# Kernel optimization log

Measured on AMD Instinct MI355X. Metric: run time of the kernel, lower is better.

Reference implementation:

```python
import jax, jax.numpy as jnp
import numpy as np

IN_F, OUT_F = 4096, 4096

def setup_inputs() -> dict:
    key = jax.random.key(0)
    k1, k2, k3, k4 = jax.random.split(key, 4)
    input = jax.random.normal(k1, (4, 2048, IN_F), dtype=jnp.float32)
    int8_weights = jax.random.randint(k2, (OUT_F, IN_F), -128, 127, dtype=jnp.int8)
    scales = jax.random.normal(k3, (OUT_F,), dtype=jnp.float32)
    bias = jax.random.normal(k4, (1, OUT_F), dtype=jnp.float32)
    return {"input": input, "int8_weights": int8_weights, "scales": scales, "bias": bias}

def reference(input, int8_weights, scales, bias):
    # dequant-then-GEMM, matching F.linear(input, W.to(dtype)) * scales + bias
    w = int8_weights.astype(input.dtype)            # [out, in]
    out = jnp.einsum('bsi,oi->bso', input, w)       # [B, S, out]
    out = out * scales                              # per-output-channel scale
    out = out + bias                                # bias broadcasts [1, out]
    return out
```

## Files before the change

kernel.cpp:

```cpp
#include <hip/hip_runtime.h>
#include <stdint.h>

typedef int   i32x4 __attribute__((ext_vector_type(4)));
typedef float f32x4 __attribute__((ext_vector_type(4)));
typedef _Float16 half8 __attribute__((ext_vector_type(8)));

#define M_DIM 8192
#define N_DIM 4096
#define K_DIM 4096
#define BM 256
#define BN 256
#define BK 64
#define NT (K_DIM / BK)
#define TILE_I8 16384

#define GLOAD_LDS16(g, l)                                        \
    __builtin_amdgcn_global_load_lds(                            \
        (const __attribute__((address_space(1))) uint32_t*)(g),  \
        (__attribute__((address_space(3))) uint32_t*)(l), 16, 0, 0)

#define BARRIER()  asm volatile("s_barrier" ::: "memory")
#define WAIT_VM0() asm volatile("s_waitcnt vmcnt(0)" ::: "memory")

__device__ __forceinline__ int img_off(int row, int slot) {
    return row * 64 + ((slot ^ ((row >> 1) & 3)) << 4);
}

__global__ __launch_bounds__(256)
void prep_a(const float* __restrict__ A, signed char* __restrict__ Apack,
            float* __restrict__ Ascale) {
    const int wv   = threadIdx.x >> 6;
    const int lane = threadIdx.x & 63;
    const int r    = blockIdx.x * 4 + wv;
    const float* row = A + (size_t)r * K_DIM;

    float mx = 0.f;
#pragma unroll
    for (int p = 0; p < 16; ++p) {
        float4 v = *(const float4*)(row + p * 256 + lane * 4);
        mx = fmaxf(mx, fmaxf(fmaxf(fabsf(v.x), fabsf(v.y)),
                             fmaxf(fabsf(v.z), fabsf(v.w))));
    }
#pragma unroll
    for (int s = 1; s < 64; s <<= 1)
        mx = fmaxf(mx, __shfl_xor(mx, s, 64));

    float inv = mx > 0.f ? 127.f / mx : 0.f;
    if (lane == 0) Ascale[r] = mx * (1.f / 127.f);

    const int bm = r >> 8, rl = r & 255;
    signed char* tb = Apack + (size_t)bm * NT * TILE_I8;
#pragma unroll
    for (int g = 0; g < 4; ++g) {
        int col0 = g * 1024 + lane * 16;
        unsigned w[4];
#pragma unroll
        for (int q = 0; q < 4; ++q) {
            float4 v = *(const float4*)(row + col0 + q * 4);
            int a0 = (int)rintf(v.x * inv);
            int a1 = (int)rintf(v.y * inv);
            int a2 = (int)rintf(v.z * inv);
            int a3 = (int)rintf(v.w * inv);
            w[q] = (a0 & 255) | ((a1 & 255) << 8) | ((a2 & 255) << 16)
                 | ((unsigned)(a3 & 255) << 24);
        }
        int kt = col0 >> 6, k = col0 & 63;
        uint4 pk = make_uint4(w[0], w[1], w[2], w[3]);
        *(uint4*)(tb + (size_t)kt * TILE_I8 + img_off(rl, k >> 4)) = pk;
    }
}

__global__ __launch_bounds__(256)
void prep_w(const void* __restrict__ Wv, signed char* __restrict__ Wpack) {
    const int* wp = (const int*)Wv;
    bool wi32 = true;
#pragma unroll
    for (int i = 0; i < 16; ++i) {
        int v = wp[i];
        wi32 = wi32 && (v >= -128 && v <= 127);
    }
    int g = blockIdx.x * 256 + threadIdx.x;
    int r = g >> 8;
    int col0 = (g & 255) << 4;
    uint4 pk;
    if (wi32) {
        const int* p = (const int*)Wv + (size_t)r * K_DIM + col0;
        unsigned w[4];
#pragma unroll
        for (int q = 0; q < 4; ++q) {
            int4 v = *(const int4*)(p + q * 4);
            w[q] = (v.x & 255) | ((v.y & 255) << 8) | ((v.z & 255) << 16)
                 | ((unsigned)(v.w & 255) << 24);
        }
        pk = make_uint4(w[0], w[1], w[2], w[3]);
    } else {
        pk = *(const uint4*)((const signed char*)Wv + (size_t)r * K_DIM + col0);
    }
    int bn = r >> 8, rl = r & 255;
    int kt = col0 >> 6, k = col0 & 63;
    *(uint4*)(Wpack + (size_t)(bn * NT + kt) * TILE_I8 + img_off(rl, k >> 4)) = pk;
}

__global__ __launch_bounds__(512, 2)
void w8a16_gemm_i8(const signed char* __restrict__ Apack,
                   const signed char* __restrict__ Wpack,
                   const float* __restrict__ Ascale,
                   const float* __restrict__ scales,
                   const float* __restrict__ bias,
                   float* __restrict__ out) {
    __shared__ char smem[65536];

    const int tid  = threadIdx.x;
    const int lane = tid & 63;
    const int wv   = tid >> 6;
    const int wm   = wv >> 2;
    const int wn   = wv & 3;
    const int r16  = lane & 15;
    const int kq   = lane >> 4;

    int bid = blockIdx.x;
    int swz = (bid & 7) * 64 + (bid >> 3);
    int bm = swz >> 4;
    int bn = swz & 15;

    const char* Abase = (const char*)Apack + (size_t)bm * NT * TILE_I8 + tid * 16;
    const char* Bbase = (const char*)Wpack + (size_t)bn * NT * TILE_I8 + tid * 16;

    auto issueT = [&](int kt_src, int buf) {
        const char* ga = Abase + (size_t)kt_src * TILE_I8;
        const char* gb = Bbase + (size_t)kt_src * TILE_I8;
        char* la = smem + buf * 32768 + tid * 16;
        char* lb = la + 16384;
        GLOAD_LDS16(ga,        la);
        GLOAD_LDS16(ga + 8192, la + 8192);
        GLOAD_LDS16(gb,        lb);
        GLOAD_LDS16(gb + 8192, lb + 8192);
    };

    i32x4 af[4], bf[4];
    i32x4 acc[8][4] = {};

    auto loadA = [&](int buf, int mh) {
#pragma unroll
        for (int m = 0; m < 4; ++m) {
            int row = wm * 128 + mh * 64 + m * 16 + r16;
            af[m] = *(const i32x4*)(smem + buf * 32768 + img_off(row, kq));
        }
    };
    auto loadB = [&](int buf) {
#pragma unroll
        for (int n = 0; n < 4; ++n) {
            int row = wn * 64 + n * 16 + r16;
            bf[n] = *(const i32x4*)(smem + buf * 32768 + 16384 + img_off(row, kq));
        }
    };
    auto mmac4 = [&](i32x4 (*ac)[4]) {
#pragma unroll
        for (int n = 0; n < 4; ++n)
#pragma unroll
            for (int m = 0; m < 4; ++m)
                ac[m][n] = __builtin_amdgcn_mfma_i32_16x16x64_i8(af[m], bf[n], ac[m][n], 0, 0, 0);
    };

    issueT(0, 0);
    WAIT_VM0();
    BARRIER();

#pragma unroll 1
    for (int t = 0; t < NT; ++t) {
        int buf  = t & 1;
        int nbuf = buf ^ 1;

        if (t + 1 < NT) issueT(t + 1, nbuf);

        loadA(buf, 0);
        loadB(buf);
        __builtin_amdgcn_s_setprio(1);
        mmac4(&acc[0]);
        __builtin_amdgcn_s_setprio(0);

        loadA(buf, 1);
        __builtin_amdgcn_s_setprio(1);
        mmac4(&acc[4]);
        __builtin_amdgcn_s_setprio(0);

        WAIT_VM0();
        BARRIER();
    }

    float sc[4], bs[4];
#pragma unroll
    for (int n = 0; n < 4; ++n) {
        int col = bn * BN + wn * 64 + n * 16 + r16;
        sc[n] = scales[col];
        bs[n] = bias[col];
    }
#pragma unroll
    for (int mi = 0; mi < 8; ++mi) {
        int row0 = bm * BM + wm * 128 + mi * 16 + kq * 4;
#pragma unroll
        for (int j = 0; j < 4; ++j) {
            int row = row0 + j;
            float as_ = Ascale[row];
#pragma unroll
            for (int n = 0; n < 4; ++n) {
                int col = bn * BN + wn * 64 + n * 16 + r16;
                out[(size_t)row * N_DIM + col] =
                    (float)acc[mi][n][j] * (as_ * sc[n]) + bs[n];
            }
        }
    }
}

__global__ __launch_bounds__(256, 2)
void w8a16_gemm(const float* __restrict__ A,
                const void* __restrict__ Wv,
                const float* __restrict__ scales,
                const float* __restrict__ bias,
                float* __restrict__ out) {
    __shared__ char smem[2 * 128 * 64 * 2];
    char* Ash = smem;
    char* Bsh = smem + 128 * 64 * 2;

    const int* wprobe = (const int*)Wv;
    bool wi32 = true;
#pragma unroll
    for (int i = 0; i < 16; ++i) {
        int v = wprobe[i];
        wi32 = wi32 && (v >= -128 && v <= 127);
    }

    const int tid  = threadIdx.x;
    const int lane = tid & 63;
    const int wv   = tid >> 6;
    const int wwm  = wv >> 1;
    const int wwn  = wv & 1;
    const int r16  = lane & 15;
    const int kq   = lane >> 4;
    const int swzl = (r16 & 7) << 4;

    int bid = blockIdx.x;
    int swz = (bid & 7) * 256 + (bid >> 3);
    int bm = swz / 32;
    int bn = swz % 32;

    const int row_a0 = bm * 128;
    const int row_b0 = bn * 128;

    int cr[4], cc[4];
#pragma unroll
    for (int i = 0; i < 4; ++i) {
        int c = tid + 256 * i;
        cr[i] = c >> 3;
        cc[i] = (c & 7) << 3;
    }

    float4 pa[8];
    int4   pbi[8];
    uint2  pb8[4];

    auto load_tile = [&](int kt) {
        int k0 = kt * 64;
#pragma unroll
        for (int i = 0; i < 4; ++i) {
            const float* p = A + (size_t)(row_a0 + cr[i]) * K_DIM + k0 + cc[i];
            pa[2 * i]     = *(const float4*)p;
            pa[2 * i + 1] = *(const float4*)(p + 4);
        }
        if (wi32) {
            const int* w = (const int*)Wv;
#pragma unroll
            for (int i = 0; i < 4; ++i) {
                const int* p = w + (size_t)(row_b0 + cr[i]) * K_DIM + k0 + cc[i];
                pbi[2 * i]     = *(const int4*)p;
                pbi[2 * i + 1] = *(const int4*)(p + 4);
            }
        } else {
            const signed char* w = (const signed char*)Wv;
#pragma unroll
            for (int i = 0; i < 4; ++i) {
                const signed char* p = w + (size_t)(row_b0 + cr[i]) * K_DIM + k0 + cc[i];
                pb8[i] = *(const uint2*)p;
            }
        }
    };

    auto write_lds = [&]() {
#pragma unroll
        for (int i = 0; i < 4; ++i) {
            int off = (cr[i] * 128 + cc[i] * 2) ^ ((cr[i] & 7) << 4);
            half8 h;
            h[0] = (_Float16)pa[2 * i].x;
            h[1] = (_Float16)pa[2 * i].y;
            h[2] = (_Float16)pa[2 * i].z;
            h[3] = (_Float16)pa[2 * i].w;
            h[4] = (_Float16)pa[2 * i + 1].x;
            h[5] = (_Float16)pa[2 * i + 1].y;
            h[6] = (_Float16)pa[2 * i + 1].z;
            h[7] = (_Float16)pa[2 * i + 1].w;
            *(half8*)(Ash + off) = h;

            half8 g;
            if (wi32) {
                g[0] = (_Float16)pbi[2 * i].x;
                g[1] = (_Float16)pbi[2 * i].y;
                g[2] = (_Float16)pbi[2 * i].z;
                g[3] = (_Float16)pbi[2 * i].w;
                g[4] = (_Float16)pbi[2 * i + 1].x;
                g[5] = (_Float16)pbi[2 * i + 1].y;
                g[6] = (_Float16)pbi[2 * i + 1].z;
                g[7] = (_Float16)pbi[2 * i + 1].w;
            } else {
                unsigned x = pb8[i].x, y = pb8[i].y;
                g[0] = (_Float16)(int)(signed char)(x & 0xff);
                g[1] = (_Float16)(int)(signed char)((x >> 8) & 0xff);
                g[2] = (_Float16)(int)(signed char)((x >> 16) & 0xff);
                g[3] = (_Float16)(int)(signed char)(x >> 24);
                g[4] = (_Float16)(int)(signed char)(y & 0xff);
                g[5] = (_Float16)(int)(signed char)((y >> 8) & 0xff);
                g[6] = (_Float16)(int)(signed char)((y >> 16) & 0xff);
                g[7] = (_Float16)(int)(signed char)(y >> 24);
            }
            *(half8*)(Bsh + off) = g;
        }
    };

    f32x4 acc[4][4] = {};

    auto compute = [&]() {
#pragma unroll
        for (int ks = 0; ks < 2; ++ks) {
            half8 af[4], bfr[4];
#pragma unroll
            for (int m = 0; m < 4; ++m) {
                int row = wwm * 64 + m * 16 + r16;
                af[m] = *(const half8*)(Ash + ((row * 128 + ks * 64 + kq * 16) ^ swzl));
            }
#pragma unroll
            for (int n = 0; n < 4; ++n) {
                int row = wwn * 64 + n * 16 + r16;
                bfr[n] = *(const half8*)(Bsh + ((row * 128 + ks * 64 + kq * 16) ^ swzl));
            }
#pragma unroll
            for (int m = 0; m < 4; ++m)
#pragma unroll
                for (int n = 0; n < 4; ++n)
                    acc[m][n] = __builtin_amdgcn_mfma_f32_16x16x32_f16(af[m], bfr[n], acc[m][n], 0, 0, 0);
        }
    };

    load_tile(0);
#pragma unroll 1
    for (int kt = 0; kt < NT; ++kt) {
        if (kt) __syncthreads();
        write_lds();
        __syncthreads();
        if (kt + 1 < NT) load_tile(kt + 1);
        compute();
    }

#pragma unroll
    for (int n = 0; n < 4; ++n) {
        int col = row_b0 + wwn * 64 + n * 16 + r16;
        float s = scales[col];
        float b = bias[col];
#pragma unroll
        for (int m = 0; m < 4; ++m) {
            int row0 = row_a0 + wwm * 64 + m * 16 + kq * 4;
#pragma unroll
            for (int j = 0; j < 4; ++j) {
                out[(size_t)(row0 + j) * N_DIM + col] = acc[m][n][j] * s + b;
            }
        }
    }
}

extern "C" void kernel_launch(void* const* d_in, const int* in_sizes, int n_in,
                              void* d_out, int out_size, void* d_ws, size_t ws_size,
                              hipStream_t stream) {
    const float* A      = (const float*)d_in[0];
    const void*  W      = d_in[1];
    const float* scales = (const float*)d_in[2];
    const float* bias   = (const float*)d_in[3];
    float*       out    = (float*)d_out;

    const size_t needA = (size_t)M_DIM * K_DIM;
    const size_t needW = (size_t)N_DIM * K_DIM;
    const size_t needS = (size_t)M_DIM * sizeof(float);

    if (ws_size >= needA + needW + needS) {
        signed char* Apack = (signed char*)d_ws;
        signed char* Wpack = (signed char*)d_ws + needA;
        float*       Asc   = (float*)((char*)d_ws + needA + needW);
        hipLaunchKernelGGL(prep_a, dim3(2048), dim3(256), 0, stream, A, Apack, Asc);
        hipLaunchKernelGGL(prep_w, dim3(4096), dim3(256), 0, stream, W, Wpack);
        hipLaunchKernelGGL(w8a16_gemm_i8, dim3(512), dim3(512), 0, stream,
                           Apack, Wpack, Asc, scales, bias, out);
    } else {
        hipLaunchKernelGGL(w8a16_gemm, dim3(2048), dim3(256), 0, stream,
                           A, W, scales, bias, out);
    }
}
```

Measured before the change: 200.2 us.

## Load int8 weight fragments straight to registers and shrink GEMM tile to 256x128

Changes the int8 GEMM tile from 256x256 with 8 waves to 256x128 with 4 waves. The weight fragments are now loaded directly from global memory into registers in an MFMA-friendly packed layout, produced by a reworked prep_w. Only the activations are staged through LDS, with double buffering and B registers prefetched one step ahead. The intent is to halve LDS traffic and footprint and raise the block count. The trade-off is more global reads of A, since each A tile is now read by twice as many column blocks, plus higher register pressure from two B fragment sets and eight A fragments.

```diff
diff --git a/kernel.cpp b/kernel.cpp
--- a/kernel.cpp
+++ b/kernel.cpp
@@ -8,11 +8,9 @@
 #define M_DIM 8192
 #define N_DIM 4096
 #define K_DIM 4096
-#define BM 256
-#define BN 256
-#define BK 64
-#define NT (K_DIM / BK)
-#define TILE_I8 16384
+#define NT 64
+#define TILE_A 16384
+#define TILE_B 8192
 
 #define GLOAD_LDS16(g, l)                                        \
     __builtin_amdgcn_global_load_lds(                            \
@@ -49,7 +47,7 @@
     if (lane == 0) Ascale[r] = mx * (1.f / 127.f);
 
     const int bm = r >> 8, rl = r & 255;
-    signed char* tb = Apack + (size_t)bm * NT * TILE_I8;
+    signed char* tb = Apack + (size_t)bm * NT * TILE_A;
 #pragma unroll
     for (int g = 0; g < 4; ++g) {
         int col0 = g * 1024 + lane * 16;
@@ -66,7 +64,7 @@
         }
         int kt = col0 >> 6, k = col0 & 63;
         uint4 pk = make_uint4(w[0], w[1], w[2], w[3]);
-        *(uint4*)(tb + (size_t)kt * TILE_I8 + img_off(rl, k >> 4)) = pk;
+        *(uint4*)(tb + (size_t)kt * TILE_A + img_off(rl, k >> 4)) = pk;
     }
 }
 
@@ -96,115 +94,114 @@
     } else {
         pk = *(const uint4*)((const signed char*)Wv + (size_t)r * K_DIM + col0);
     }
-    int bn = r >> 8, rl = r & 255;
+    int bn = r >> 7, rl = r & 127;
     int kt = col0 >> 6, k = col0 & 63;
-    *(uint4*)(Wpack + (size_t)(bn * NT + kt) * TILE_I8 + img_off(rl, k >> 4)) = pk;
-}
-
-__global__ __launch_bounds__(512, 2)
+    *(uint4*)(Wpack + ((size_t)(bn * NT + kt) * 128 + rl) * 64 + k) = pk;
+}
+
+__global__ __launch_bounds__(256, 2)
 void w8a16_gemm_i8(const signed char* __restrict__ Apack,
                    const signed char* __restrict__ Wpack,
                    const float* __restrict__ Ascale,
                    const float* __restrict__ scales,
                    const float* __restrict__ bias,
                    float* __restrict__ out) {
-    __shared__ char smem[65536];
+    __shared__ char smem[32768];
 
     const int tid  = threadIdx.x;
     const int lane = tid & 63;
     const int wv   = tid >> 6;
-    const int wm   = wv >> 2;
-    const int wn   = wv & 3;
+    const int wm   = wv >> 1;
+    const int wn   = wv & 1;
     const int r16  = lane & 15;
     const int kq   = lane >> 4;
 
     int bid = blockIdx.x;
-    int swz = (bid & 7) * 64 + (bid >> 3);
-    int bm = swz >> 4;
-    int bn = swz & 15;
-
-    const char* Abase = (const char*)Apack + (size_t)bm * NT * TILE_I8 + tid * 16;
-    const char* Bbase = (const char*)Wpack + (size_t)bn * NT * TILE_I8 + tid * 16;
-
-    auto issueT = [&](int kt_src, int buf) {
-        const char* ga = Abase + (size_t)kt_src * TILE_I8;
-        const char* gb = Bbase + (size_t)kt_src * TILE_I8;
-        char* la = smem + buf * 32768 + tid * 16;
-        char* lb = la + 16384;
-        GLOAD_LDS16(ga,        la);
-        GLOAD_LDS16(ga + 8192, la + 8192);
-        GLOAD_LDS16(gb,        lb);
-        GLOAD_LDS16(gb + 8192, lb + 8192);
-    };
-
-    i32x4 af[4], bf[4];
+    int swz = (bid & 7) * 128 + (bid >> 3);
+    int bn = swz >> 5;
+    int bm = swz & 31;
+
+    const char* Abase = (const char*)Apack + (size_t)bm * NT * TILE_A + tid * 16;
+    const char* Bfrag = (const char*)Wpack + (size_t)bn * NT * TILE_B
+                      + (wn * 64 + r16) * 64 + kq * 16;
+
+    auto stageA = [&](int kt, int buf) {
+        const char* ga = Abase + (size_t)kt * TILE_A;
+        char* la = smem + buf * 16384 + tid * 16;
+        GLOAD_LDS16(ga,          la);
+        GLOAD_LDS16(ga + 4096,   la + 4096);
+        GLOAD_LDS16(ga + 8192,   la + 8192);
+        GLOAD_LDS16(ga + 12288,  la + 12288);
+    };
+    auto loadB = [&](int kt, i32x4 (&b)[4]) {
+        const char* gb = Bfrag + (size_t)kt * TILE_B;
+#pragma unroll
+        for (int n = 0; n < 4; ++n)
+            b[n] = *(const i32x4*)(gb + n * 1024);
+    };
+
     i32x4 acc[8][4] = {};
 
-    auto loadA = [&](int buf, int mh) {
-#pragma unroll
-        for (int m = 0; m < 4; ++m) {
-            int row = wm * 128 + mh * 64 + m * 16 + r16;
-            af[m] = *(const i32x4*)(smem + buf * 32768 + img_off(row, kq));
-        }
-    };
-    auto loadB = [&](int buf) {
-#pragma unroll
-        for (int n = 0; n < 4; ++n) {
-            int row = wn * 64 + n * 16 + r16;
-            bf[n] = *(const i32x4*)(smem + buf * 32768 + 16384 + img_off(row, kq));
-        }
-    };
-    auto mmac4 = [&](i32x4 (*ac)[4]) {
+    auto compute = [&](int buf, i32x4 (&bf)[4]) {
+        i32x4 af[8];
+#pragma unroll
+        for (int m = 0; m < 8; ++m) {
+            int row = wm * 128 + m * 16 + r16;
+            af[m] = *(const i32x4*)(smem + buf * 16384 + img_off(row, kq));
+        }
+        __builtin_amdgcn_s_setprio(1);
 #pragma unroll
         for (int n = 0; n < 4; ++n)
 #pragma unroll
-            for (int m = 0; m < 4; ++m)
-                ac[m][n] = __builtin_amdgcn_mfma_i32_16x16x64_i8(af[m], bf[n], ac[m][n], 0, 0, 0);
-    };
-
-    issueT(0, 0);
+            for (int m = 0; m < 8; ++m)
+                acc[m][n] = __builtin_amdgcn_mfma_i32_16x16x64_i8(af[m], bf[n], acc[m][n], 0, 0, 0);
+        __builtin_amdgcn_s_setprio(0);
+    };
+
+    i32x4 bf0[4], bf1[4];
+
+    loadB(0, bf0);
+    stageA(0, 0);
     WAIT_VM0();
     BARRIER();
 
 #pragma unroll 1
-    for (int t = 0; t < NT; ++t) {
-        int buf  = t & 1;
-        int nbuf = buf ^ 1;
-
-        if (t + 1 < NT) issueT(t + 1, nbuf);
-
-        loadA(buf, 0);
-        loadB(buf);
-        __builtin_amdgcn_s_setprio(1);
-        mmac4(&acc[0]);
-        __builtin_amdgcn_s_setprio(0);
-
-        loadA(buf, 1);
-        __builtin_amdgcn_s_setprio(1);
-        mmac4(&acc[4]);
-        __builtin_amdgcn_s_setprio(0);
-
-        WAIT_VM0();
-        BARRIER();
+    for (int t = 0; t < NT; t += 2) {
+        {
+            int tn = (t + 1 < NT) ? t + 1 : NT - 1;
+            loadB(tn, bf1);
+            stageA(tn, 1);
+            compute(0, bf0);
+            WAIT_VM0();
+            BARRIER();
+        }
+        {
+            int tn = (t + 2 < NT) ? t + 2 : NT - 1;
+            loadB(tn, bf0);
+            stageA(tn, 0);
+            compute(1, bf1);
+            WAIT_VM0();
+            BARRIER();
+        }
     }
 
     float sc[4], bs[4];
 #pragma unroll
     for (int n = 0; n < 4; ++n) {
-        int col = bn * BN + wn * 64 + n * 16 + r16;
+        int col = bn * 128 + wn * 64 + n * 16 + r16;
         sc[n] = scales[col];
         bs[n] = bias[col];
     }
 #pragma unroll
     for (int mi = 0; mi < 8; ++mi) {
-        int row0 = bm * BM + wm * 128 + mi * 16 + kq * 4;
+        int row0 = bm * 256 + wm * 128 + mi * 16 + kq * 4;
 #pragma unroll
         for (int j = 0; j < 4; ++j) {
             int row = row0 + j;
             float as_ = Ascale[row];
 #pragma unroll
             for (int n = 0; n < 4; ++n) {
-                int col = bn * BN + wn * 64 + n * 16 + r16;
+                int col = bn * 128 + wn * 64 + n * 16 + r16;
                 out[(size_t)row * N_DIM + col] =
                     (float)acc[mi][n][j] * (as_ * sc[n]) + bs[n];
             }
@@ -394,7 +391,7 @@
         float*       Asc   = (float*)((char*)d_ws + needA + needW);
         hipLaunchKernelGGL(prep_a, dim3(2048), dim3(256), 0, stream, A, Apack, Asc);
         hipLaunchKernelGGL(prep_w, dim3(4096), dim3(256), 0, stream, W, Wpack);
-        hipLaunchKernelGGL(w8a16_gemm_i8, dim3(512), dim3(512), 0, stream,
+        hipLaunchKernelGGL(w8a16_gemm_i8, dim3(1024), dim3(256), 0, stream,
                            Apack, Wpack, Asc, scales, bias, out);
     } else {
         hipLaunchKernelGGL(w8a16_gemm, dim3(2048), dim3(256), 0, stream,
```

After: 213.7 us. 1.07x slower.
